# Kernel optimization log

Hardware: AMD Instinct MI355X
Metric: run time of the kernel (lower is better)

The kernel has to match this reference:

```python
import jax, jax.numpy as jnp
import numpy as np

B, T, NIN = 128, 256, 16
H1 = H2 = 512
NACT = 4
SLOPE = 25.0  # snntorch FastSigmoid default slope

@jax.custom_vjp
def spike(x):
    return (x > 0).astype(x.dtype)

def _spike_fwd(x):
    return (x > 0).astype(x.dtype), x

def _spike_bwd(x, g):
    # FastSigmoid surrogate: d/dx = 1 / (slope*|x| + 1)^2
    return (g / (SLOPE * jnp.abs(x) + 1.0) ** 2,)

spike.defvjp(_spike_fwd, _spike_bwd)

def setup_inputs() -> dict:
    key = jax.random.key(0)
    ks = jax.random.split(key, 12)
    def lin(k, fan_in, shape):
        lim = 1.0 / np.sqrt(fan_in)
        return jax.random.uniform(k, shape, jnp.float32, -lim, lim)
    return {
        "batch": jax.random.uniform(ks[0], (B, T, NIN), jnp.float32, 0.0, 2.5),
        "W1": lin(ks[1], NIN, (H1, NIN)), "b1": lin(ks[2], NIN, (H1,)),
        "beta1": jax.random.uniform(ks[3], (H1,), jnp.float32),
        "thr1": jax.random.uniform(ks[4], (H1,), jnp.float32),
        "W2": lin(ks[5], H1, (H2, H1)), "b2": lin(ks[6], H1, (H2,)),
        "beta2": jax.random.uniform(ks[7], (H2,), jnp.float32),
        "thr2": jax.random.uniform(ks[8], (H2,), jnp.float32),
        "Wa": lin(ks[9], H2, (NACT, H2)), "ba": lin(ks[10], H2, (NACT,)),
        "beta_act": jnp.float32(0.95),
        "inp_min": jnp.float32(0.0),
        "inp_max": jnp.float32(2.5),
    }

def _lif_subtract(cur, mem, beta, thr):
    # snntorch Leaky: reset from PRE-update membrane, detached; subtract reset
    reset = jax.lax.stop_gradient((mem - thr > 0).astype(mem.dtype))
    mem = jnp.clip(beta, 0.0, 1.0) * mem + cur - reset * thr
    return spike(mem - thr), mem

def reference(batch, W1, b1, beta1, thr1, W2, b2, beta2, thr2, Wa, ba, beta_act, inp_min, inp_max):
    Bb = batch.shape[0]
    x_seq = jnp.swapaxes(batch, 0, 1)  # [T, B, NIN]
    mem1 = jnp.zeros((Bb, W1.shape[0]), batch.dtype)
    mem2 = jnp.zeros((Bb, W2.shape[0]), batch.dtype)
    mem_a = jnp.zeros((Bb, Wa.shape[0]), batch.dtype)

    def step(carry, x):
        mem1, mem2, mem_a = carry
        x = (x - inp_min) / (inp_max - inp_min)
        spk1, mem1 = _lif_subtract(x @ W1.T + b1, mem1, beta1, thr1)
        spk2, mem2 = _lif_subtract(spk1 @ W2.T + b2, mem2, beta2, thr2)
        act = spk2 @ Wa.T + ba
        # action_lif: reset_mechanism='none', beta=0.95 learnable
        mem_a = jnp.clip(beta_act, 0.0, 1.0) * mem_a + act
        return (mem1, mem2, mem_a), mem_a.reshape(-1)  # torch: mem_act.reshape((1,-1))

    _, vals = jax.lax.scan(step, (mem1, mem2, mem_a), x_seq)
    # torch.stack(values, dim=1) of (1, B*NACT) tensors -> (1, T, B*NACT)
    return vals[None, :, :]
```

## Files before the change

### kernel.cpp

```cpp
#include <hip/hip_runtime.h>
#include <stdint.h>

typedef __attribute__((ext_vector_type(8))) short short8;
typedef __attribute__((ext_vector_type(4))) float f32x4;

#define T_STEPS 256
#define BATCH   128

#define LDS_BARRIER() asm volatile("s_waitcnt lgkmcnt(0)\n\ts_barrier" ::: "memory")

static __device__ inline unsigned short f2bf(float f) {
    unsigned int u = __float_as_uint(f);
    unsigned int r = u + 0x7FFFu + ((u >> 16) & 1u);
    return (unsigned short)(r >> 16);
}
static __device__ inline unsigned pack_hi16(unsigned a, unsigned b) {
    return __builtin_amdgcn_perm(b, a, 0x07060302u);
}
static __device__ inline void gload_lds16(const unsigned short* g, unsigned short* l) {
    __builtin_amdgcn_global_load_lds(
        (const __attribute__((address_space(1))) unsigned int*)(const void*)g,
        (__attribute__((address_space(3))) unsigned int*)(void*)l,
        16, 0, 0);
}

__global__ __launch_bounds__(256) void k_prep(
    const float* __restrict__ W2, const float* __restrict__ W1,
    const float* __restrict__ b1, const float* __restrict__ thr1,
    const float* __restrict__ imin_p, const float* __restrict__ imax_p,
    const float* __restrict__ batch,
    unsigned short* __restrict__ W2hi, unsigned short* __restrict__ W2lo,
    unsigned short* __restrict__ W1rows, float* __restrict__ b1s,
    unsigned short* __restrict__ Xf)
{
    int blk = blockIdx.x, tid = threadIdx.x;
    if (blk < 256) {
        int gid = blk * 256 + tid;
        f32x4 wv = *(const f32x4*)(W2 + (size_t)gid * 4);
        unsigned short hi[4], lo[4];
#pragma unroll
        for (int e = 0; e < 4; ++e) {
            float wf = wv[e];
            unsigned short h = f2bf(wf);
            float hf = __uint_as_float(((unsigned int)h) << 16);
            hi[e] = h;
            lo[e] = f2bf(wf - hf);
        }
        uint2 ph, pl;
        ph.x = (unsigned)hi[0] | ((unsigned)hi[1] << 16);
        ph.y = (unsigned)hi[2] | ((unsigned)hi[3] << 16);
        pl.x = (unsigned)lo[0] | ((unsigned)lo[1] << 16);
        pl.y = (unsigned)lo[2] | ((unsigned)lo[3] << 16);
        *(uint2*)(W2hi + (size_t)gid * 4) = ph;
        *(uint2*)(W2lo + (size_t)gid * 4) = pl;
    } else if (blk < 258) {
        int h = (blk - 256) * 256 + tid;
        float wsc = 1.0f / thr1[h];
        unsigned short row[64];
#pragma unroll
        for (int k = 0; k < 16; ++k) {
            float wv = W1[h * 16 + k] * wsc;
            unsigned a = __float_as_uint(wv) & 0xFFFF0000u;
            float r1 = wv - __uint_as_float(a);
            unsigned m = __float_as_uint(r1) & 0xFFFF0000u;
            float r2 = r1 - __uint_as_float(m);
            unsigned l = __float_as_uint(r2) & 0xFFFF0000u;
            row[k]      = (unsigned short)(a >> 16);
            row[16 + k] = (unsigned short)(m >> 16);
            row[32 + k] = (unsigned short)(l >> 16);
            row[48 + k] = 0;
        }
        b1s[h] = b1[h] * wsc;
        uint4* dst = (uint4*)(W1rows + (size_t)h * 64);
#pragma unroll
        for (int i = 0; i < 8; ++i) dst[i] = ((uint4*)row)[i];
    } else {
        int gid    = (blk - 258) * 256 + tid;
        int lane32 = gid & 31;
        int btile  = (gid >> 5) & 7;
        int t      = gid >> 8;
        int q1 = lane32 >> 4, m15 = lane32 & 15;
        int b  = btile * 16 + m15;
        float imin = imin_p[0];
        float isc  = 1.0f / (imax_p[0] - imin);
        const float* xp = batch + ((size_t)b * T_STEPS + t) * 16 + q1 * 8;
        unsigned uh[8], um[8], ul[8];
#pragma unroll
        for (int j = 0; j < 8; ++j) {
            float xv = (xp[j] - imin) * isc;
            unsigned a = __float_as_uint(xv) & 0xFFFF0000u;
            float r1 = xv - __uint_as_float(a);
            unsigned m = __float_as_uint(r1) & 0xFFFF0000u;
            float r2 = r1 - __uint_as_float(m);
            unsigned l = __float_as_uint(r2) & 0xFFFF0000u;
            uh[j] = a; um[j] = m; ul[j] = l;
        }
        uint4 XH, XM, XL;
        XH.x = pack_hi16(uh[0], uh[1]); XH.y = pack_hi16(uh[2], uh[3]);
        XH.z = pack_hi16(uh[4], uh[5]); XH.w = pack_hi16(uh[6], uh[7]);
        XM.x = pack_hi16(um[0], um[1]); XM.y = pack_hi16(um[2], um[3]);
        XM.z = pack_hi16(um[4], um[5]); XM.w = pack_hi16(um[6], um[7]);
        XL.x = pack_hi16(ul[0], ul[1]); XL.y = pack_hi16(ul[2], ul[3]);
        XL.z = pack_hi16(ul[4], ul[5]); XL.w = pack_hi16(ul[6], ul[7]);
        unsigned short* dst = Xf + ((size_t)t * 8 + btile) * 1024 + lane32 * 8;
        *(uint4*)(dst +   0) = XH;
        *(uint4*)(dst + 256) = XM;
        *(uint4*)(dst + 512) = XL;
    }
}

union XF { uint4 u; short8 s; };

__global__ __launch_bounds__(1024, 4) void k_main(
    const unsigned short* __restrict__ Xf,
    const unsigned short* __restrict__ W2hi, const unsigned short* __restrict__ W2lo,
    const unsigned short* __restrict__ W1rows, const float* __restrict__ b1s,
    const float* __restrict__ beta1, const float* __restrict__ b2,
    const float* __restrict__ beta2, const float* __restrict__ thr2,
    unsigned short* __restrict__ spkbits)
{
    __shared__ unsigned short Aw[8192];
    __shared__ float Cbuf[4][4096];
    __shared__ unsigned short Xs[8192];

    int tid  = threadIdx.x;
    int lane = tid & 63;
    int w    = tid >> 6;
    int q = lane >> 4, m15 = lane & 15;
    int btile = blockIdx.x & 7;
    int slice = blockIdx.x >> 3;

    short8 A1[2], A2[2], A3[2];
#pragma unroll
    for (int c = 0; c < 2; ++c) {
        const unsigned short* rp = W1rows + (size_t)(w * 32 + c * 16 + m15) * 64;
        A1[c] = *(const short8*)(rp + q * 8);
        A2[c] = *(const short8*)(rp + q * 8 + (q >> 1) * 16);
        A3[c] = *(const short8*)(rp + 16 + q * 8);
    }
    int jg = slice * 16 + m15;
    short8 bhi = *(const short8*)(W2hi + (size_t)jg * 512 + w * 32 + q * 8);
    short8 blo = *(const short8*)(W2lo + (size_t)jg * 512 + w * 32 + q * 8);

    f32x4 b14[2], bet1[2];
#pragma unroll
    for (int c = 0; c < 2; ++c) {
        int h0 = w * 32 + c * 16 + q * 4;
        b14[c] = *(const f32x4*)(b1s + h0);
        f32x4 bb = *(const f32x4*)(beta1 + h0);
#pragma unroll
        for (int r = 0; r < 4; ++r) bet1[c][r] = fminf(fmaxf(bb[r], 0.0f), 1.0f);
    }
    float m1[8], spk1f[8];
#pragma unroll
    for (int i = 0; i < 8; ++i) { m1[i] = 0.0f; spk1f[i] = 0.0f; }

    float beta2r = fminf(fmaxf(beta2[jg], 0.0f), 1.0f);
    float thr2r  = thr2[jg];
    float nthr2  = -thr2r;
    float b2r    = b2[jg];
    float m2 = 0.0f, spk2f = 0.0f;

    const unsigned short* xgbase = Xf + (size_t)btile * 1024 + (size_t)lane * 8;
    int l31x8 = (lane & 31) * 8;
    int o1 = l31x8;
    int o2 = l31x8 + 256;
    int o3 = l31x8 + (lane < 32 ? 512 : 0);
    int o4 = l31x8 + (lane < 32 ? 512 : 256);

    unsigned short* myAw = Aw + w * 512;
    int wr0 = (0 * 2 + (q >> 1)) * 128 + (m15 ^ (q >> 1)) * 8 + (q & 1) * 4;
    int wr1 = (1 * 2 + (q >> 1)) * 128 + (m15 ^ (q >> 1)) * 8 + (q & 1) * 4;
    int rdo = (q * 16 + (m15 ^ (q & 1))) * 8;

    if (w == 15) {
#pragma unroll
        for (int s = 0; s < 4; ++s) {
            gload_lds16(xgbase + (size_t)s * 8192,       Xs + s * 1024);
            gload_lds16(xgbase + (size_t)s * 8192 + 512, Xs + s * 1024 + 512);
        }
        asm volatile("s_waitcnt vmcnt(0)" ::: "memory");
    }
    __syncthreads();

    XF xc[4], xn[4];
    {
        const unsigned short* s = Xs;
        xc[0].u = *(const uint4*)(s + o1);
        xc[1].u = *(const uint4*)(s + o2);
        xc[2].u = *(const uint4*)(s + o3);
        xc[3].u = *(const uint4*)(s + o4);
    }

    auto reduce_one = [&](int slot, int step) __attribute__((always_inline)) {
        float cur2 = b2r;
#pragma unroll
        for (int wp = 0; wp < 16; ++wp) cur2 += Cbuf[slot][w * 1024 + wp * 64 + lane];
        m2 = fmaf(beta2r, m2, cur2);
        m2 = fmaf(spk2f, nthr2, m2);
        bool sp2 = m2 > thr2r;
        spk2f = sp2 ? 1.0f : 0.0f;
        unsigned long long mask = __ballot(sp2);
        if (lane < 4) {
            unsigned short v = (unsigned short)(mask >> (lane * 16));
            spkbits[((size_t)step * BATCH + btile * 16 + lane * 4 + w) * 32 + slice] = v;
        }
    };

    auto gbody = [&](int ts, int k, XF* xcur, XF* xnx) __attribute__((always_inline)) {
        if (((k & 1) == 0) && w == 15) {
            int ta = ts + k + 4; if (ta > T_STEPS - 1) ta = T_STEPS - 1;
            int tb = ts + k + 5; if (tb > T_STEPS - 1) tb = T_STEPS - 1;
            const unsigned short* ga = xgbase + (size_t)ta * 8192;
            const unsigned short* gb = xgbase + (size_t)tb * 8192;
            unsigned short* la = Xs + ((k + 4) & 7) * 1024;
            unsigned short* lb = Xs + ((k + 5) & 7) * 1024;
            gload_lds16(ga,       la);
            gload_lds16(ga + 512, la + 512);
            gload_lds16(gb,       lb);
            gload_lds16(gb + 512, lb + 512);
        }
        {
            const unsigned short* sx = Xs + ((k + 1) & 7) * 1024;
            xnx[0].u = *(const uint4*)(sx + o1);
            xnx[1].u = *(const uint4*)(sx + o2);
            xnx[2].u = *(const uint4*)(sx + o3);
            xnx[3].u = *(const uint4*)(sx + o4);
        }
        f32x4 D[2];
#pragma unroll
        for (int c = 0; c < 2; ++c) {
            D[c] = __builtin_amdgcn_mfma_f32_16x16x32_bf16(A1[c], xcur[0].s, b14[c], 0, 0, 0);
            D[c] = __builtin_amdgcn_mfma_f32_16x16x32_bf16(A1[c], xcur[1].s, D[c], 0, 0, 0);
            D[c] = __builtin_amdgcn_mfma_f32_16x16x32_bf16(A2[c], xcur[2].s, D[c], 0, 0, 0);
            D[c] = __builtin_amdgcn_mfma_f32_16x16x32_bf16(A3[c], xcur[3].s, D[c], 0, 0, 0);
        }
#pragma unroll
        for (int i = 0; i < 8; ++i) {
            int c = i >> 2, r = i & 3;
            float mv = fmaf(bet1[c][r], m1[i], D[c][r]);
            mv -= spk1f[i];
            bool sp = mv > 1.0f;
            m1[i] = mv;
            spk1f[i] = sp ? 1.0f : 0.0f;
        }
        {
            uint2 pk0, pk1;
            pk0.x = pack_hi16(__float_as_uint(spk1f[0]), __float_as_uint(spk1f[1]));
            pk0.y = pack_hi16(__float_as_uint(spk1f[2]), __float_as_uint(spk1f[3]));
            pk1.x = pack_hi16(__float_as_uint(spk1f[4]), __float_as_uint(spk1f[5]));
            pk1.y = pack_hi16(__float_as_uint(spk1f[6]), __float_as_uint(spk1f[7]));
            *(uint2*)(myAw + wr0) = pk0;
            *(uint2*)(myAw + wr1) = pk1;
        }
        union { uint4 u; short8 s; } af;
        af.u = *(uint4*)(myAw + rdo);
        f32x4 C2 = { 0.f, 0.f, 0.f, 0.f };
        C2 = __builtin_amdgcn_mfma_f32_16x16x32_bf16(af.s, bhi, C2, 0, 0, 0);
        C2 = __builtin_amdgcn_mfma_f32_16x16x32_bf16(af.s, blo, C2, 0, 0, 0);
        float* cb = Cbuf[k & 3];
#pragma unroll
        for (int r = 0; r < 4; ++r)
            cb[r * 1024 + w * 64 + lane] = C2[r];
        if (k & 1) {
            if (w == 15) asm volatile("s_waitcnt vmcnt(0)" ::: "memory");
            LDS_BARRIER();
        }
    };

#pragma unroll 1
    for (int ts = 0; ts < T_STEPS; ts += 8) {
#pragma unroll
        for (int kk = 0; kk < 4; ++kk) {
            int k = kk * 2;
            if (w < 4 && (ts + k >= 2)) {
                reduce_one((k + 2) & 3, ts + k - 2);
                reduce_one((k + 3) & 3, ts + k - 1);
            }
            gbody(ts, k,     xc, xn);
            gbody(ts, k + 1, xn, xc);
        }
    }
    if (w < 4) {
        reduce_one(2, T_STEPS - 2);
        reduce_one(3, T_STEPS - 1);
    }
}

__global__ __launch_bounds__(512) void k_act(
    const unsigned short* __restrict__ spkbits,
    const float* __restrict__ Wa, const float* __restrict__ ba,
    const float* __restrict__ beta_act_p, float* __restrict__ out,
    f32x4* __restrict__ Lws, f32x4* __restrict__ Cws)
{
    __shared__ f32x4 waT[512];
    __shared__ f32x4 part[512];
    __shared__ f32x4 sc[128];
    int tid = threadIdx.x;
    int b   = blockIdx.x & 127;
    int c   = blockIdx.x >> 7;
    int tl  = tid & 127;
    int s   = tid >> 7;
    int t   = c * 128 + tl;

    {
        f32x4 v = { Wa[tid], Wa[512 + tid], Wa[1024 + tid], Wa[1536 + tid] };
        waT[tid] = v;
    }
    float bact = fminf(fmaxf(beta_act_p[0], 0.0f), 1.0f);
    f32x4 acc;
    if (s == 0) { acc[0] = ba[0]; acc[1] = ba[1]; acc[2] = ba[2]; acc[3] = ba[3]; }
    else        { acc[0] = 0.f;   acc[1] = 0.f;   acc[2] = 0.f;   acc[3] = 0.f;   }
    __syncthreads();

    const unsigned short* sp = spkbits + ((size_t)t * BATCH + b) * 32 + s * 8;
    uint4 v = *(const uint4*)sp;
    unsigned int wbuf[4] = { v.x, v.y, v.z, v.w };
#pragma unroll
    for (int ww = 0; ww < 4; ++ww) {
#pragma unroll
        for (int half = 0; half < 2; ++half) {
            unsigned int wd = (wbuf[ww] >> (half * 16)) & 0xFFFFu;
            int seg = s * 8 + ww * 2 + half;
#pragma unroll
            for (int i = 0; i < 16; ++i) {
                float sel = ((wd >> i) & 1u) ? 1.0f : 0.0f;
                f32x4 wv = waT[seg * 16 + i];
                acc[0] = fmaf(sel, wv[0], acc[0]);
                acc[1] = fmaf(sel, wv[1], acc[1]);
                acc[2] = fmaf(sel, wv[2], acc[2]);
                acc[3] = fmaf(sel, wv[3], acc[3]);
            }
        }
    }
    part[tid] = acc;
    __syncthreads();
    if (tid < 128) {
        f32x4 a0 = part[tid], a1 = part[tid + 128], a2 = part[tid + 256], a3 = part[tid + 384];
        f32x4 sum;
        sum[0] = ((a0[0] + a1[0]) + a2[0]) + a3[0];
        sum[1] = ((a0[1] + a1[1]) + a2[1]) + a3[1];
        sum[2] = ((a0[2] + a1[2]) + a2[2]) + a3[2];
        sum[3] = ((a0[3] + a1[3]) + a2[3]) + a3[3];
        sc[tid] = sum;
    }
    __syncthreads();
    float bd = bact;
    for (int d = 1; d < 128; d <<= 1) {
        f32x4 cv = { 0.f, 0.f, 0.f, 0.f }, pv = { 0.f, 0.f, 0.f, 0.f };
        if (tid < 128) {
            cv = sc[tid];
            if (tid >= d) pv = sc[tid - d];
        }
        __syncthreads();
        if (tid < 128) {
            cv[0] = fmaf(bd, pv[0], cv[0]);
            cv[1] = fmaf(bd, pv[1], cv[1]);
            cv[2] = fmaf(bd, pv[2], cv[2]);
            cv[3] = fmaf(bd, pv[3], cv[3]);
            sc[tid] = cv;
        }
        __syncthreads();
        bd *= bd;
    }
    if (tid < 128) {
        f32x4 res = sc[tid];
        if (c == 0) {
            *(f32x4*)(out + (size_t)t * 512 + b * 4) = res;
            if (tl == 127) Cws[b] = res;
        } else {
            Lws[b * 128 + tl] = res;
        }
    }
}

__global__ __launch_bounds__(128) void k_act2(
    const f32x4* __restrict__ Lws, const f32x4* __restrict__ Cws,
    const float* __restrict__ beta_act_p, float* __restrict__ out)
{
    int tl = threadIdx.x;
    int b  = blockIdx.x;
    float bact = fminf(fmaxf(beta_act_p[0], 0.0f), 1.0f);
    float p = 1.0f, base = bact;
    int e = tl + 1;
#pragma unroll
    for (int i = 0; i < 8; ++i) { if (e & 1) p *= base; base *= base; e >>= 1; }
    f32x4 L = Lws[b * 128 + tl];
    f32x4 C = Cws[b];
    f32x4 r;
    r[0] = fmaf(p, C[0], L[0]);
    r[1] = fmaf(p, C[1], L[1]);
    r[2] = fmaf(p, C[2], L[2]);
    r[3] = fmaf(p, C[3], L[3]);
    *(f32x4*)(out + (size_t)(128 + tl) * 512 + b * 4) = r;
}

extern "C" void kernel_launch(void* const* d_in, const int* in_sizes, int n_in,
                              void* d_out, int out_size, void* d_ws, size_t ws_size,
                              hipStream_t stream)
{
    const float* batch    = (const float*)d_in[0];
    const float* W1       = (const float*)d_in[1];
    const float* b1       = (const float*)d_in[2];
    const float* beta1    = (const float*)d_in[3];
    const float* thr1     = (const float*)d_in[4];
    const float* W2       = (const float*)d_in[5];
    const float* b2       = (const float*)d_in[6];
    const float* beta2    = (const float*)d_in[7];
    const float* thr2     = (const float*)d_in[8];
    const float* Wa       = (const float*)d_in[9];
    const float* ba       = (const float*)d_in[10];
    const float* beta_act = (const float*)d_in[11];
    const float* inp_min  = (const float*)d_in[12];
    const float* inp_max  = (const float*)d_in[13];
    float* out            = (float*)d_out;

    char* ws = (char*)d_ws;
    unsigned short* W2hi    = (unsigned short*)ws;
    unsigned short* W2lo    = (unsigned short*)(ws + (512u << 10));
    unsigned short* W1rows  = (unsigned short*)(ws + (1u << 20));
    float*          b1s     = (float*)(ws + (1u << 20) + (64u << 10));
    unsigned short* Xf      = (unsigned short*)(ws + (2u << 20));
    f32x4*          Lws     = (f32x4*)(ws + (6u << 20));
    f32x4*          Cws     = (f32x4*)(ws + (6u << 20) + (256u << 10));
    unsigned short* spkbits = (unsigned short*)(ws + (10u << 20));

    hipLaunchKernelGGL(k_prep, dim3(514), dim3(256), 0, stream,
                       W2, W1, b1, thr1, inp_min, inp_max, batch,
                       W2hi, W2lo, W1rows, b1s, Xf);
    hipLaunchKernelGGL(k_main, dim3(256), dim3(1024), 0, stream,
                       Xf, W2hi, W2lo, W1rows, b1s, beta1, b2, beta2, thr2, spkbits);
    hipLaunchKernelGGL(k_act, dim3(256), dim3(512), 0, stream,
                       spkbits, Wa, ba, beta_act, out, Lws, Cws);
    hipLaunchKernelGGL(k_act2, dim3(128), dim3(128), 0, stream, Lws, Cws, beta_act, out);
}
```

Before: 258.7 us.

## Load per-step input fragments directly from global instead of LDS staging ring

Removes the LDS ring buffer that one wave filled via global_load_lds several steps ahead. Each wave now reads its next-step input fragments straight from global memory, one step ahead in registers, and the vmcnt wait in the barrier path is dropped. This saves 16KB of LDS and the producer-wave work and wait, but the global-load latency now sits on the critical path of a serial time loop with only a one-step prefetch. The outer loop is also shortened to four steps per iteration.

```diff
diff --git a/kernel.cpp b/kernel.cpp
--- a/kernel.cpp
+++ b/kernel.cpp
@@ -16,12 +16,6 @@
 }
 static __device__ inline unsigned pack_hi16(unsigned a, unsigned b) {
     return __builtin_amdgcn_perm(b, a, 0x07060302u);
-}
-static __device__ inline void gload_lds16(const unsigned short* g, unsigned short* l) {
-    __builtin_amdgcn_global_load_lds(
-        (const __attribute__((address_space(1))) unsigned int*)(const void*)g,
-        (__attribute__((address_space(3))) unsigned int*)(void*)l,
-        16, 0, 0);
 }
 
 __global__ __launch_bounds__(256) void k_prep(
@@ -121,7 +115,6 @@
 {
     __shared__ unsigned short Aw[8192];
     __shared__ float Cbuf[4][4096];
-    __shared__ unsigned short Xs[8192];
 
     int tid  = threadIdx.x;
     int lane = tid & 63;
@@ -161,7 +154,7 @@
     float b2r    = b2[jg];
     float m2 = 0.0f, spk2f = 0.0f;
 
-    const unsigned short* xgbase = Xf + (size_t)btile * 1024 + (size_t)lane * 8;
+    const unsigned short* xg = Xf + (size_t)btile * 1024;
     int l31x8 = (lane & 31) * 8;
     int o1 = l31x8;
     int o2 = l31x8 + 256;
@@ -173,19 +166,9 @@
     int wr1 = (1 * 2 + (q >> 1)) * 128 + (m15 ^ (q >> 1)) * 8 + (q & 1) * 4;
     int rdo = (q * 16 + (m15 ^ (q & 1))) * 8;
 
-    if (w == 15) {
-#pragma unroll
-        for (int s = 0; s < 4; ++s) {
-            gload_lds16(xgbase + (size_t)s * 8192,       Xs + s * 1024);
-            gload_lds16(xgbase + (size_t)s * 8192 + 512, Xs + s * 1024 + 512);
-        }
-        asm volatile("s_waitcnt vmcnt(0)" ::: "memory");
-    }
-    __syncthreads();
-
     XF xc[4], xn[4];
     {
-        const unsigned short* s = Xs;
+        const unsigned short* s = xg;
         xc[0].u = *(const uint4*)(s + o1);
         xc[1].u = *(const uint4*)(s + o2);
         xc[2].u = *(const uint4*)(s + o3);
@@ -208,20 +191,9 @@
     };
 
     auto gbody = [&](int ts, int k, XF* xcur, XF* xnx) __attribute__((always_inline)) {
-        if (((k & 1) == 0) && w == 15) {
-            int ta = ts + k + 4; if (ta > T_STEPS - 1) ta = T_STEPS - 1;
-            int tb = ts + k + 5; if (tb > T_STEPS - 1) tb = T_STEPS - 1;
-            const unsigned short* ga = xgbase + (size_t)ta * 8192;
-            const unsigned short* gb = xgbase + (size_t)tb * 8192;
-            unsigned short* la = Xs + ((k + 4) & 7) * 1024;
-            unsigned short* lb = Xs + ((k + 5) & 7) * 1024;
-            gload_lds16(ga,       la);
-            gload_lds16(ga + 512, la + 512);
-            gload_lds16(gb,       lb);
-            gload_lds16(gb + 512, lb + 512);
-        }
         {
-            const unsigned short* sx = Xs + ((k + 1) & 7) * 1024;
+            int tn = ts + k + 1; if (tn > T_STEPS - 1) tn = T_STEPS - 1;
+            const unsigned short* sx = xg + (size_t)tn * 8192;
             xnx[0].u = *(const uint4*)(sx + o1);
             xnx[1].u = *(const uint4*)(sx + o2);
             xnx[2].u = *(const uint4*)(sx + o3);
@@ -263,15 +235,14 @@
         for (int r = 0; r < 4; ++r)
             cb[r * 1024 + w * 64 + lane] = C2[r];
         if (k & 1) {
-            if (w == 15) asm volatile("s_waitcnt vmcnt(0)" ::: "memory");
             LDS_BARRIER();
         }
     };
 
 #pragma unroll 1
-    for (int ts = 0; ts < T_STEPS; ts += 8) {
-#pragma unroll
-        for (int kk = 0; kk < 4; ++kk) {
+    for (int ts = 0; ts < T_STEPS; ts += 4) {
+#pragma unroll
+        for (int kk = 0; kk < 2; ++kk) {
             int k = kk * 2;
             if (w < 4 && (ts + k >= 2)) {
                 reduce_one((k + 2) & 3, ts + k - 2);
```

New measurement: 278.0 us. +7.5%, slower.

## Halve LDS staging of inputs, read rest from global, consolidate layer-2 reduction into one wave

Applied to the files above, without the earlier changes.

Only half of each timestep's input tile is staged into LDS via async global-to-LDS loads. The other half is read directly from global memory by every wave, which shrinks the Xs buffer and the DMA issue work. Partial layer-2 results are now written as one vectorized f32x4 store into a swizzled layout, so a single wave can reduce all four rows with vector LDS reads, where previously four waves each did scalar reads. This lowers LDS traffic and removes reduction work from waves 1-3, but it adds global-load latency to the critical per-step path and puts the whole reduction on one wave.

```diff
diff --git a/kernel.cpp b/kernel.cpp
--- a/kernel.cpp
+++ b/kernel.cpp
@@ -121,7 +121,7 @@
 {
     __shared__ unsigned short Aw[8192];
     __shared__ float Cbuf[4][4096];
-    __shared__ unsigned short Xs[8192];
+    __shared__ unsigned short Xs[4096];
 
     int tid  = threadIdx.x;
     int lane = tid & 63;
@@ -159,9 +159,11 @@
     float thr2r  = thr2[jg];
     float nthr2  = -thr2r;
     float b2r    = b2[jg];
-    float m2 = 0.0f, spk2f = 0.0f;
+    float m2a[4]   = { 0.0f, 0.0f, 0.0f, 0.0f };
+    float spk2a[4] = { 0.0f, 0.0f, 0.0f, 0.0f };
 
     const unsigned short* xgbase = Xf + (size_t)btile * 1024 + (size_t)lane * 8;
+    const unsigned short* xg     = Xf + (size_t)btile * 1024;
     int l31x8 = (lane & 31) * 8;
     int o1 = l31x8;
     int o2 = l31x8 + 256;
@@ -173,37 +175,50 @@
     int wr1 = (1 * 2 + (q >> 1)) * 128 + (m15 ^ (q >> 1)) * 8 + (q & 1) * 4;
     int rdo = (q * 16 + (m15 ^ (q & 1))) * 8;
 
+    int cwo = q * 1024 + m15 * 64 + (((w ^ m15) & 15) << 2);
+
     if (w == 15) {
 #pragma unroll
-        for (int s = 0; s < 4; ++s) {
-            gload_lds16(xgbase + (size_t)s * 8192,       Xs + s * 1024);
-            gload_lds16(xgbase + (size_t)s * 8192 + 512, Xs + s * 1024 + 512);
-        }
+        for (int s = 0; s < 4; ++s)
+            gload_lds16(xgbase + (size_t)s * 8192, Xs + s * 512);
         asm volatile("s_waitcnt vmcnt(0)" ::: "memory");
     }
     __syncthreads();
 
     XF xc[4], xn[4];
     {
-        const unsigned short* s = Xs;
-        xc[0].u = *(const uint4*)(s + o1);
-        xc[1].u = *(const uint4*)(s + o2);
-        xc[2].u = *(const uint4*)(s + o3);
-        xc[3].u = *(const uint4*)(s + o4);
+        xc[0].u = *(const uint4*)(Xs + o1);
+        xc[1].u = *(const uint4*)(Xs + o2);
+        xc[2].u = *(const uint4*)(xg + o3);
+        xc[3].u = *(const uint4*)(xg + o4);
     }
 
     auto reduce_one = [&](int slot, int step) __attribute__((always_inline)) {
-        float cur2 = b2r;
-#pragma unroll
-        for (int wp = 0; wp < 16; ++wp) cur2 += Cbuf[slot][w * 1024 + wp * 64 + lane];
-        m2 = fmaf(beta2r, m2, cur2);
-        m2 = fmaf(spk2f, nthr2, m2);
-        bool sp2 = m2 > thr2r;
-        spk2f = sp2 ? 1.0f : 0.0f;
-        unsigned long long mask = __ballot(sp2);
-        if (lane < 4) {
-            unsigned short v = (unsigned short)(mask >> (lane * 16));
-            spkbits[((size_t)step * BATCH + btile * 16 + lane * 4 + w) * 32 + slice] = v;
+        const float* cb = &Cbuf[slot][q * 1024 + m15 * 64];
+        f32x4 acc = { b2r, b2r, b2r, b2r };
+#pragma unroll
+        for (int wp = 0; wp < 16; ++wp) {
+            f32x4 v = *(const f32x4*)(cb + (((wp ^ m15) & 15) << 2));
+            acc[0] += v[0]; acc[1] += v[1]; acc[2] += v[2]; acc[3] += v[3];
+        }
+        unsigned long long msk[4];
+#pragma unroll
+        for (int r = 0; r < 4; ++r) {
+            float mv = fmaf(beta2r, m2a[r], acc[r]);
+            mv = fmaf(spk2a[r], nthr2, mv);
+            bool sp = mv > thr2r;
+            m2a[r] = mv;
+            spk2a[r] = sp ? 1.0f : 0.0f;
+            msk[r] = __ballot(sp);
+        }
+        if (lane < 16) {
+            int rr = lane & 3, bqs = lane >> 2;
+            unsigned long long mm = msk[0];
+            mm = (rr == 1) ? msk[1] : mm;
+            mm = (rr == 2) ? msk[2] : mm;
+            mm = (rr == 3) ? msk[3] : mm;
+            unsigned short v = (unsigned short)(mm >> (bqs * 16));
+            spkbits[((size_t)step * BATCH + btile * 16 + lane) * 32 + slice] = v;
         }
     };
 
@@ -211,21 +226,17 @@
         if (((k & 1) == 0) && w == 15) {
             int ta = ts + k + 4; if (ta > T_STEPS - 1) ta = T_STEPS - 1;
             int tb = ts + k + 5; if (tb > T_STEPS - 1) tb = T_STEPS - 1;
-            const unsigned short* ga = xgbase + (size_t)ta * 8192;
-            const unsigned short* gb = xgbase + (size_t)tb * 8192;
-            unsigned short* la = Xs + ((k + 4) & 7) * 1024;
-            unsigned short* lb = Xs + ((k + 5) & 7) * 1024;
-            gload_lds16(ga,       la);
-            gload_lds16(ga + 512, la + 512);
-            gload_lds16(gb,       lb);
-            gload_lds16(gb + 512, lb + 512);
+            gload_lds16(xgbase + (size_t)ta * 8192, Xs + ((k + 4) & 7) * 512);
+            gload_lds16(xgbase + (size_t)tb * 8192, Xs + ((k + 5) & 7) * 512);
         }
         {
-            const unsigned short* sx = Xs + ((k + 1) & 7) * 1024;
-            xnx[0].u = *(const uint4*)(sx + o1);
-            xnx[1].u = *(const uint4*)(sx + o2);
-            xnx[2].u = *(const uint4*)(sx + o3);
-            xnx[3].u = *(const uint4*)(sx + o4);
+            int tn = ts + k + 1; if (tn > T_STEPS - 1) tn = T_STEPS - 1;
+            const unsigned short* sl = Xs + ((k + 1) & 7) * 512;
+            const unsigned short* sg = xg + (size_t)tn * 8192;
+            xnx[0].u = *(const uint4*)(sl + o1);
+            xnx[1].u = *(const uint4*)(sl + o2);
+            xnx[2].u = *(const uint4*)(sg + o3);
+            xnx[3].u = *(const uint4*)(sg + o4);
         }
         f32x4 D[2];
 #pragma unroll
@@ -258,10 +269,7 @@
         f32x4 C2 = { 0.f, 0.f, 0.f, 0.f };
         C2 = __builtin_amdgcn_mfma_f32_16x16x32_bf16(af.s, bhi, C2, 0, 0, 0);
         C2 = __builtin_amdgcn_mfma_f32_16x16x32_bf16(af.s, blo, C2, 0, 0, 0);
-        float* cb = Cbuf[k & 3];
-#pragma unroll
-        for (int r = 0; r < 4; ++r)
-            cb[r * 1024 + w * 64 + lane] = C2[r];
+        *(f32x4*)(&Cbuf[k & 3][cwo]) = C2;
         if (k & 1) {
             if (w == 15) asm volatile("s_waitcnt vmcnt(0)" ::: "memory");
             LDS_BARRIER();
@@ -273,7 +281,7 @@
 #pragma unroll
         for (int kk = 0; kk < 4; ++kk) {
             int k = kk * 2;
-            if (w < 4 && (ts + k >= 2)) {
+            if (w == 0 && (ts + k >= 2)) {
                 reduce_one((k + 2) & 3, ts + k - 2);
                 reduce_one((k + 3) & 3, ts + k - 1);
             }
@@ -281,7 +289,7 @@
             gbody(ts, k + 1, xn, xc);
         }
     }
-    if (w < 4) {
+    if (w == 0) {
         reduce_one(2, T_STEPS - 2);
         reduce_one(3, T_STEPS - 1);
     }
```

New measurement: 942.9 us. 264% more time.

## Batch four timesteps per barrier with eight-slot partial-sum ring

Applied to the files above, without the earlier changes.

Restructures the main recurrent loop so that a workgroup barrier happens once every four timesteps instead of every two. The layer-2 partial-sum buffer grows from four to eight slots, and the X prefetch issues four timesteps per group. The reduction waves then process four delayed steps at once. This halves the barrier count on the serial critical path, at the cost of doubling Cbuf LDS use (which may cut occupancy) and making the reduction work burstier.

```diff
diff --git a/kernel.cpp b/kernel.cpp
--- a/kernel.cpp
+++ b/kernel.cpp
@@ -119,8 +119,8 @@
     const float* __restrict__ beta2, const float* __restrict__ thr2,
     unsigned short* __restrict__ spkbits)
 {
+    __shared__ float Cbuf[8][4096];
     __shared__ unsigned short Aw[8192];
-    __shared__ float Cbuf[4][4096];
     __shared__ unsigned short Xs[8192];
 
     int tid  = threadIdx.x;
@@ -175,7 +175,7 @@
 
     if (w == 15) {
 #pragma unroll
-        for (int s = 0; s < 4; ++s) {
+        for (int s = 0; s < 5; ++s) {
             gload_lds16(xgbase + (size_t)s * 8192,       Xs + s * 1024);
             gload_lds16(xgbase + (size_t)s * 8192 + 512, Xs + s * 1024 + 512);
         }
@@ -191,6 +191,7 @@
         xc[2].u = *(const uint4*)(s + o3);
         xc[3].u = *(const uint4*)(s + o4);
     }
+    __syncthreads();
 
     auto reduce_one = [&](int slot, int step) __attribute__((always_inline)) {
         float cur2 = b2r;
@@ -208,18 +209,6 @@
     };
 
     auto gbody = [&](int ts, int k, XF* xcur, XF* xnx) __attribute__((always_inline)) {
-        if (((k & 1) == 0) && w == 15) {
-            int ta = ts + k + 4; if (ta > T_STEPS - 1) ta = T_STEPS - 1;
-            int tb = ts + k + 5; if (tb > T_STEPS - 1) tb = T_STEPS - 1;
-            const unsigned short* ga = xgbase + (size_t)ta * 8192;
-            const unsigned short* gb = xgbase + (size_t)tb * 8192;
-            unsigned short* la = Xs + ((k + 4) & 7) * 1024;
-            unsigned short* lb = Xs + ((k + 5) & 7) * 1024;
-            gload_lds16(ga,       la);
-            gload_lds16(ga + 512, la + 512);
-            gload_lds16(gb,       lb);
-            gload_lds16(gb + 512, lb + 512);
-        }
         {
             const unsigned short* sx = Xs + ((k + 1) & 7) * 1024;
             xnx[0].u = *(const uint4*)(sx + o1);
@@ -258,32 +247,45 @@
         f32x4 C2 = { 0.f, 0.f, 0.f, 0.f };
         C2 = __builtin_amdgcn_mfma_f32_16x16x32_bf16(af.s, bhi, C2, 0, 0, 0);
         C2 = __builtin_amdgcn_mfma_f32_16x16x32_bf16(af.s, blo, C2, 0, 0, 0);
-        float* cb = Cbuf[k & 3];
+        float* cb = Cbuf[k & 7];
 #pragma unroll
         for (int r = 0; r < 4; ++r)
             cb[r * 1024 + w * 64 + lane] = C2[r];
-        if (k & 1) {
-            if (w == 15) asm volatile("s_waitcnt vmcnt(0)" ::: "memory");
-            LDS_BARRIER();
-        }
+    };
+
+    auto group = [&](int ts, int G) __attribute__((always_inline)) {
+        if (w == 15) {
+#pragma unroll
+            for (int i = 0; i < 4; ++i) {
+                int s = ts + G + 5 + i; if (s > T_STEPS - 1) s = T_STEPS - 1;
+                const unsigned short* g = xgbase + (size_t)s * 8192;
+                unsigned short* l = Xs + ((G + 5 + i) & 7) * 1024;
+                gload_lds16(g,       l);
+                gload_lds16(g + 512, l + 512);
+            }
+        }
+        if (w < 4 && (ts + G >= 4)) {
+#pragma unroll
+            for (int i = 0; i < 4; ++i)
+                reduce_one((G + 4 + i) & 7, ts + G - 4 + i);
+        }
+        gbody(ts, G + 0, xc, xn);
+        gbody(ts, G + 1, xn, xc);
+        gbody(ts, G + 2, xc, xn);
+        gbody(ts, G + 3, xn, xc);
+        if (w == 15) asm volatile("s_waitcnt vmcnt(0)" ::: "memory");
+        LDS_BARRIER();
     };
 
 #pragma unroll 1
     for (int ts = 0; ts < T_STEPS; ts += 8) {
-#pragma unroll
-        for (int kk = 0; kk < 4; ++kk) {
-            int k = kk * 2;
-            if (w < 4 && (ts + k >= 2)) {
-                reduce_one((k + 2) & 3, ts + k - 2);
-                reduce_one((k + 3) & 3, ts + k - 1);
-            }
-            gbody(ts, k,     xc, xn);
-            gbody(ts, k + 1, xn, xc);
-        }
+        group(ts, 0);
+        group(ts, 4);
     }
     if (w < 4) {
-        reduce_one(2, T_STEPS - 2);
-        reduce_one(3, T_STEPS - 1);
+#pragma unroll
+        for (int i = 0; i < 4; ++i)
+            reduce_one(4 + i, T_STEPS - 4 + i);
     }
 }
 
```

Result: no change. 258.4 us (-0.1%).
